# Kernel tuning notes

Hardware: AMD Instinct MI355X
Metric: run time of the kernel (lower is better)

The kernel has to match this reference:

```python
import jax, jax.numpy as jnp
import numpy as np

HIDDEN = 512
HEADS = 8


def setup_inputs() -> dict:
    key = jax.random.key(0)
    ks = jax.random.split(key, 7)
    B, S, D = 4, 2048, HIDDEN
    scale = 1.0 / np.sqrt(D)
    return {
        "src": jax.random.normal(ks[0], (B, S, D), dtype=jnp.float32),
        "Wq": jax.random.normal(ks[1], (D, D), dtype=jnp.float32) * scale,
        "bq": jax.random.normal(ks[2], (D,), dtype=jnp.float32) * 0.01,
        "Wk": jax.random.normal(ks[3], (D, D), dtype=jnp.float32) * scale,
        "bk": jax.random.normal(ks[4], (D,), dtype=jnp.float32) * 0.01,
        "Wv": jax.random.normal(ks[5], (D, D), dtype=jnp.float32) * scale,
        "bv": jax.random.normal(ks[6], (D,), dtype=jnp.float32) * 0.01,
    }


def reference(src, Wq, bq, Wk, bk, Wv, bv):
    B, S, D = src.shape
    H = HEADS
    hd = D // H
    # QKV projections -> [B, S, H, hd]
    q = (src @ Wq + bq).reshape(B, S, H, hd)
    k = (src @ Wk + bk).reshape(B, S, H, hd)
    v = (src @ Wv + bv).reshape(B, S, H, hd)
    # scores [B, H, S, S]; note: NO causal mask (matches original module)
    scores = jnp.einsum("bqhd,bkhd->bhqk", q, k) / jnp.sqrt(jnp.asarray(hd, src.dtype))
    attn = jax.nn.softmax(scores, axis=-1)
    out = jnp.einsum("bhqk,bkhd->bqhd", attn, v)
    return out.reshape(B, S, D)
```

## Files before the change

### kernel.cpp

```cpp
#include <hip/hip_runtime.h>

typedef __bf16 bf16;
typedef __bf16 bf16x8 __attribute__((ext_vector_type(8)));
typedef __bf16 bf16x4 __attribute__((ext_vector_type(4)));
typedef float f32x4 __attribute__((ext_vector_type(4)));
typedef float f32x16 __attribute__((ext_vector_type(16)));
typedef unsigned int u32;

#define QK_SCALE 0.1803368801111204f

__device__ __forceinline__ int swzb(int row, int col) {
    return (((row) << 7) + ((col) << 1)) ^ (((row) & 7) << 4);
}

__device__ __forceinline__ void gload_lds16(const void* g, void* l) {
    __builtin_amdgcn_global_load_lds(
        (const __attribute__((address_space(1))) unsigned int*)g,
        (__attribute__((address_space(3))) unsigned int*)l, 16, 0, 0);
}

__device__ __forceinline__ u32 cvtpk(float lo, float hi) {
    u32 r;
    asm("v_cvt_pk_bf16_f32 %0, %1, %2" : "=v"(r) : "v"(lo), "v"(hi));
    return r;
}

__device__ __forceinline__ void pl32swap(u32& a, u32& b) {
    asm("v_permlane32_swap_b32 %0, %1" : "+v"(a), "+v"(b));
}

__global__ __launch_bounds__(256) void cast_src(const float* __restrict__ x,
                                                bf16* __restrict__ y) {
    int i = blockIdx.x * 256 + threadIdx.x;
    float4 v = reinterpret_cast<const float4*>(x)[i];
    bf16x4 p;
    p[0] = (bf16)v.x; p[1] = (bf16)v.y; p[2] = (bf16)v.z; p[3] = (bf16)v.w;
    reinterpret_cast<bf16x4*>(y)[i] = p;
}

__global__ __launch_bounds__(256) void wtrans_all(const float* __restrict__ Wq,
                                                  const float* __restrict__ Wk,
                                                  const float* __restrict__ Wv,
                                                  bf16* __restrict__ Wt_all) {
    __shared__ float T[64][65];
    const int w = blockIdx.z;
    const float* W = w == 0 ? Wq : (w == 1 ? Wk : Wv);
    const float wsc = (w == 0) ? QK_SCALE : 1.0f;
    bf16* Wt = Wt_all + (size_t)w * 512 * 512;
    const int k0 = blockIdx.x * 64, n0 = blockIdx.y * 64;
    const int tx = threadIdx.x & 63, ty = threadIdx.x >> 6;
#pragma unroll
    for (int i = 0; i < 16; ++i) {
        int row = ty * 16 + i;
        T[row][tx] = W[(size_t)(k0 + row) * 512 + n0 + tx];
    }
    __syncthreads();
#pragma unroll
    for (int i = 0; i < 16; ++i) {
        int row = ty * 16 + i;
        Wt[(size_t)(n0 + row) * 512 + k0 + tx] = (bf16)(T[tx][row] * wsc);
    }
}

__global__ __launch_bounds__(256) void qkv_gemm_all(const bf16* __restrict__ srcb,
                                                    const bf16* __restrict__ Wt_all,
                                                    const float* __restrict__ bq,
                                                    const float* __restrict__ bk,
                                                    const float* __restrict__ bv,
                                                    bf16* __restrict__ Qb,
                                                    bf16* __restrict__ Kb,
                                                    bf16* __restrict__ Vtb) {
    __shared__ __align__(16) bf16 As[128 * 64];
    __shared__ __align__(16) bf16 Bs[128 * 64];
    const int t = threadIdx.x, lane = t & 63, wid = t >> 6;
    const int m0 = blockIdx.x * 128;
    const int n0g = blockIdx.y * 128;
    const int oi = n0g >> 9, n0 = n0g & 511;
    const float* bias = oi == 0 ? bq : (oi == 1 ? bk : bv);
    const float bsc = (oi == 0) ? QK_SCALE : 1.0f;
    bf16* outp = oi == 0 ? Qb : (oi == 1 ? Kb : Vtb);
    const bf16* Wt = Wt_all + (size_t)oi * 512 * 512;
    const bool sw = (oi == 2);
    const int wm = (wid >> 1) * 64, wn = (wid & 1) * 64;
    const int fr = lane & 15, fq = lane >> 4;

    f32x4 acc[4][4] = {};

    for (int k0 = 0; k0 < 512; k0 += 64) {
        __syncthreads();
#pragma unroll
        for (int c = 0; c < 4; ++c) {
            int u = (wid * 4 + c) * 64 + lane;
            int row = u >> 3;
            int slot = (u & 7) ^ (row & 7);
            gload_lds16(srcb + (size_t)(m0 + row) * 512 + k0 + slot * 8,
                        (char*)As + (wid * 4 + c) * 1024);
            gload_lds16(Wt + (size_t)(n0 + row) * 512 + k0 + slot * 8,
                        (char*)Bs + (wid * 4 + c) * 1024);
        }
        __syncthreads();

        bf16x8 a[2][4], b[2][4];
#pragma unroll
        for (int c = 0; c < 2; ++c)
#pragma unroll
            for (int i = 0; i < 4; ++i) {
                a[c][i] = *reinterpret_cast<const bf16x8*>(
                    (const char*)As + swzb(wm + i * 16 + fr, c * 32 + fq * 8));
                b[c][i] = *reinterpret_cast<const bf16x8*>(
                    (const char*)Bs + swzb(wn + i * 16 + fr, c * 32 + fq * 8));
            }
        if (!sw) {
#pragma unroll
            for (int i = 0; i < 4; ++i)
#pragma unroll
                for (int j = 0; j < 4; ++j)
#pragma unroll
                    for (int c = 0; c < 2; ++c)
                        acc[i][j] = __builtin_amdgcn_mfma_f32_16x16x32_bf16(a[c][i], b[c][j], acc[i][j], 0, 0, 0);
        } else {
#pragma unroll
            for (int i = 0; i < 4; ++i)
#pragma unroll
                for (int j = 0; j < 4; ++j)
#pragma unroll
                    for (int c = 0; c < 2; ++c)
                        acc[i][j] = __builtin_amdgcn_mfma_f32_16x16x32_bf16(b[c][j], a[c][i], acc[i][j], 0, 0, 0);
        }
    }

    if (!sw) {
#pragma unroll
        for (int j = 0; j < 4; ++j) {
            int n = n0 + wn + j * 16 + fr;
            float bj = bias[n] * bsc;
            int h = n >> 6, d = n & 63;
#pragma unroll
            for (int i = 0; i < 4; ++i)
#pragma unroll
                for (int r = 0; r < 4; ++r) {
                    int m = m0 + wm + i * 16 + fq * 4 + r;
                    int b_ = m >> 11, s = m & 2047;
                    outp[(((size_t)(b_ * 8 + h)) * 2048 + s) * 64 + d] =
                        (bf16)(acc[i][j][r] + bj);
                }
        }
    } else {
#pragma unroll
        for (int j = 0; j < 4; ++j)
#pragma unroll
            for (int r = 0; r < 4; ++r) {
                int n = n0 + wn + j * 16 + fq * 4 + r;
                float bj = bias[n];
                int h = n >> 6, d = n & 63;
#pragma unroll
                for (int i = 0; i < 4; ++i) {
                    int m = m0 + wm + i * 16 + fr;
                    int b_ = m >> 11, s = m & 2047;
                    outp[(((size_t)(b_ * 8 + h)) * 64 + d) * 2048 + s] =
                        (bf16)(acc[i][j][r] + bj);
                }
            }
    }
}

__global__ __launch_bounds__(256, 2) void attn_fwd(const bf16* __restrict__ Q,
                                                   const bf16* __restrict__ K,
                                                   const bf16* __restrict__ Vt,
                                                   float* __restrict__ out) {
    __shared__ __align__(16) bf16 Ks[2][64 * 64];
    __shared__ __align__(16) bf16 Vs[2][64 * 64];
    const int t = threadIdx.x, lane = t & 63, wid = t >> 6;
    const int c31 = lane & 31, h = lane >> 5;
    const int bh = blockIdx.y;
    const int qw = blockIdx.x * 128 + wid * 32;

    const bf16* Qp = Q + ((size_t)bh * 2048 + qw + c31) * 64;
    bf16x8 qf[4];
#pragma unroll
    for (int ks = 0; ks < 4; ++ks)
        qf[ks] = *reinterpret_cast<const bf16x8*>(&Qp[ks * 16 + h * 8]);

    bf16x8 bones;
#pragma unroll
    for (int e = 0; e < 8; ++e) bones[e] = (bf16)1.0f;

    f32x16 acc_o[2] = {};
    f32x16 acc_l = {};

    const char* Kpb0 = (const char*)(K + (size_t)bh * 2048 * 64);
    const char* Vpb0 = (const char*)(Vt + (size_t)bh * 64 * 2048);

    const int u0 = wid * 2 * 64 + lane, u1 = u0 + 64;
    const int row0 = u0 >> 3, slot0 = (u0 & 7) ^ (row0 & 7);
    const int row1 = u1 >> 3, slot1 = (u1 & 7) ^ (row1 & 7);

    auto stage = [&](int buf, int kv0) {
        const char* Kpb = Kpb0 + (size_t)kv0 * 128;
        const char* Vpb = Vpb0 + (size_t)kv0 * 2;
        gload_lds16(Kpb + row0 * 128 + slot0 * 16, (char*)Ks[buf] + (wid * 2 + 0) * 1024);
        gload_lds16(Kpb + row1 * 128 + slot1 * 16, (char*)Ks[buf] + (wid * 2 + 1) * 1024);
        gload_lds16(Vpb + (size_t)row0 * 4096 + slot0 * 16, (char*)Vs[buf] + (wid * 2 + 0) * 1024);
        gload_lds16(Vpb + (size_t)row1 * 4096 + slot1 * 16, (char*)Vs[buf] + (wid * 2 + 1) * 1024);
    };

    auto compute = [&](int buf) {
        f32x16 s[2] = {};
#pragma unroll
        for (int kt = 0; kt < 2; ++kt)
#pragma unroll
            for (int ks = 0; ks < 4; ++ks) {
                bf16x8 kf = *reinterpret_cast<const bf16x8*>(
                    (const char*)Ks[buf] + swzb(kt * 32 + c31, ks * 16 + h * 8));
                s[kt] = __builtin_amdgcn_mfma_f32_32x32x16_bf16(kf, qf[ks], s[kt], 0, 0, 0);
            }

#pragma unroll
        for (int kt = 0; kt < 2; ++kt)
#pragma unroll
            for (int r = 0; r < 16; ++r)
                s[kt][r] = exp2f(s[kt][r]);

        bf16x8 pa[4];
#pragma unroll
        for (int kt = 0; kt < 2; ++kt)
#pragma unroll
            for (int k2 = 0; k2 < 2; ++k2) {
                u32 X = cvtpk(s[kt][8 * k2 + 0], s[kt][8 * k2 + 1]);
                u32 Y = cvtpk(s[kt][8 * k2 + 4], s[kt][8 * k2 + 5]);
                u32 Z = cvtpk(s[kt][8 * k2 + 2], s[kt][8 * k2 + 3]);
                u32 W = cvtpk(s[kt][8 * k2 + 6], s[kt][8 * k2 + 7]);
                pl32swap(X, Y);
                pl32swap(Z, W);
                union { bf16x8 v; u32 w[4]; } pu;
                pu.w[0] = X; pu.w[1] = Z; pu.w[2] = Y; pu.w[3] = W;
                pa[kt * 2 + k2] = pu.v;
            }

#pragma unroll
        for (int kstep = 0; kstep < 4; ++kstep) {
#pragma unroll
            for (int dt = 0; dt < 2; ++dt) {
                bf16x8 vf = *reinterpret_cast<const bf16x8*>(
                    (const char*)Vs[buf] + swzb(dt * 32 + c31, kstep * 16 + h * 8));
                acc_o[dt] = __builtin_amdgcn_mfma_f32_32x32x16_bf16(pa[kstep], vf, acc_o[dt], 0, 0, 0);
            }
            acc_l = __builtin_amdgcn_mfma_f32_32x32x16_bf16(pa[kstep], bones, acc_l, 0, 0, 0);
        }
    };

    stage(0, 0);
    __syncthreads();

    for (int kv0 = 0; kv0 < 2048; kv0 += 128) {
        stage(1, kv0 + 64);
        compute(0);
        __syncthreads();
        if (kv0 + 128 < 2048) stage(0, kv0 + 128);
        compute(1);
        __syncthreads();
    }

    const int b_ = bh >> 3, hh = bh & 7;
#pragma unroll
    for (int reg = 0; reg < 16; ++reg) {
        float inv = __builtin_amdgcn_rcpf(acc_l[reg]);
        int qr = (reg & 3) + 8 * (reg >> 2) + 4 * h;
        int s_ = qw + qr;
        size_t base = ((size_t)b_ * 2048 + s_) * 512 + hh * 64;
        out[base + c31]      = acc_o[0][reg] * inv;
        out[base + 32 + c31] = acc_o[1][reg] * inv;
    }
}

extern "C" void kernel_launch(void* const* d_in, const int* in_sizes, int n_in,
                              void* d_out, int out_size, void* d_ws, size_t ws_size,
                              hipStream_t stream) {
    const float* src = (const float*)d_in[0];
    const float* Wq  = (const float*)d_in[1];
    const float* bq  = (const float*)d_in[2];
    const float* Wk  = (const float*)d_in[3];
    const float* bk  = (const float*)d_in[4];
    const float* Wv  = (const float*)d_in[5];
    const float* bv  = (const float*)d_in[6];
    float* out = (float*)d_out;

    char* ws = (char*)d_ws;
    const size_t WT_SZ  = 512u * 512u * sizeof(bf16);
    const size_t QKV_SZ = 8192u * 512u * sizeof(bf16);
    bf16* WtA  = (bf16*)(ws);
    bf16* srcb = (bf16*)(ws + 3 * WT_SZ);
    bf16* Qb   = (bf16*)(ws + 3 * WT_SZ + QKV_SZ);
    bf16* Kb   = (bf16*)(ws + 3 * WT_SZ + 2 * QKV_SZ);
    bf16* Vtb  = (bf16*)(ws + 3 * WT_SZ + 3 * QKV_SZ);

    cast_src<<<4096, 256, 0, stream>>>(src, srcb);
    wtrans_all<<<dim3(8, 8, 3), 256, 0, stream>>>(Wq, Wk, Wv, WtA);

    qkv_gemm_all<<<dim3(64, 12), 256, 0, stream>>>(srcb, WtA, bq, bk, bv, Qb, Kb, Vtb);

    attn_fwd<<<dim3(16, 32), 256, 0, stream>>>(Qb, Kb, Vtb, out);
}
```

Baseline: 94.93 us.

## Double KV tile per stage in attention and add MFMA priority hints

The attention kernel now stages 128 KV rows per buffer instead of 64, which halves the number of barriers and loop iterations. It adds a new XOR swizzle for the wider V tile (16-way over 256-byte rows). Inside compute, the two score tiles are interleaved and wrapped with s_setprio, and exp2 now uses the raw builtin. LDS use doubles to 64KB per block, which may limit occupancy at the 2 blocks per CU the launch bounds request.

```diff
diff --git a/kernel.cpp b/kernel.cpp
--- a/kernel.cpp
+++ b/kernel.cpp
@@ -12,6 +12,12 @@
 __device__ __forceinline__ int swzb(int row, int col) {
     return (((row) << 7) + ((col) << 1)) ^ (((row) & 7) << 4);
 }
+__device__ __forceinline__ int kswz(int row, int g) {
+    return row * 128 + ((g ^ (row & 7)) << 4);
+}
+__device__ __forceinline__ int vswz(int row, int g) {
+    return row * 256 + ((g ^ (row & 15)) << 4);
+}
 
 __device__ __forceinline__ void gload_lds16(const void* g, void* l) {
     __builtin_amdgcn_global_load_lds(
@@ -24,7 +30,6 @@
     asm("v_cvt_pk_bf16_f32 %0, %1, %2" : "=v"(r) : "v"(lo), "v"(hi));
     return r;
 }
-
 __device__ __forceinline__ void pl32swap(u32& a, u32& b) {
     asm("v_permlane32_swap_b32 %0, %1" : "+v"(a), "+v"(b));
 }
@@ -168,8 +173,8 @@
                                                    const bf16* __restrict__ K,
                                                    const bf16* __restrict__ Vt,
                                                    float* __restrict__ out) {
-    __shared__ __align__(16) bf16 Ks[2][64 * 64];
-    __shared__ __align__(16) bf16 Vs[2][64 * 64];
+    __shared__ __align__(16) bf16 Ks[2][128 * 64];
+    __shared__ __align__(16) bf16 Vs[2][64 * 128];
     const int t = threadIdx.x, lane = t & 63, wid = t >> 6;
     const int c31 = lane & 31, h = lane >> 5;
     const int bh = blockIdx.y;
@@ -191,72 +196,91 @@
     const char* Kpb0 = (const char*)(K + (size_t)bh * 2048 * 64);
     const char* Vpb0 = (const char*)(Vt + (size_t)bh * 64 * 2048);
 
-    const int u0 = wid * 2 * 64 + lane, u1 = u0 + 64;
-    const int row0 = u0 >> 3, slot0 = (u0 & 7) ^ (row0 & 7);
-    const int row1 = u1 >> 3, slot1 = (u1 & 7) ^ (row1 & 7);
+    int koffs[4], voffs[4];
+#pragma unroll
+    for (int c = 0; c < 4; ++c) {
+        int cc = wid * 4 + c;
+        int kr = cc * 8 + (lane >> 3);
+        koffs[c] = kr * 128 + (((lane & 7) ^ (kr & 7)) << 4);
+        int d = cc * 4 + (lane >> 4);
+        voffs[c] = d * 4096 + (((lane & 15) ^ (d & 15)) << 4);
+    }
 
     auto stage = [&](int buf, int kv0) {
-        const char* Kpb = Kpb0 + (size_t)kv0 * 128;
-        const char* Vpb = Vpb0 + (size_t)kv0 * 2;
-        gload_lds16(Kpb + row0 * 128 + slot0 * 16, (char*)Ks[buf] + (wid * 2 + 0) * 1024);
-        gload_lds16(Kpb + row1 * 128 + slot1 * 16, (char*)Ks[buf] + (wid * 2 + 1) * 1024);
-        gload_lds16(Vpb + (size_t)row0 * 4096 + slot0 * 16, (char*)Vs[buf] + (wid * 2 + 0) * 1024);
-        gload_lds16(Vpb + (size_t)row1 * 4096 + slot1 * 16, (char*)Vs[buf] + (wid * 2 + 1) * 1024);
+#pragma unroll
+        for (int c = 0; c < 4; ++c)
+            gload_lds16(Kpb0 + (size_t)kv0 * 128 + koffs[c],
+                        (char*)Ks[buf] + (wid * 4 + c) * 1024);
+#pragma unroll
+        for (int c = 0; c < 4; ++c)
+            gload_lds16(Vpb0 + (size_t)kv0 * 2 + voffs[c],
+                        (char*)Vs[buf] + (wid * 4 + c) * 1024);
     };
 
     auto compute = [&](int buf) {
-        f32x16 s[2] = {};
-#pragma unroll
-        for (int kt = 0; kt < 2; ++kt)
+#pragma unroll
+        for (int p = 0; p < 2; ++p) {
+            f32x16 s0 = {}, s1 = {};
+            __builtin_amdgcn_s_setprio(1);
 #pragma unroll
             for (int ks = 0; ks < 4; ++ks) {
-                bf16x8 kf = *reinterpret_cast<const bf16x8*>(
-                    (const char*)Ks[buf] + swzb(kt * 32 + c31, ks * 16 + h * 8));
-                s[kt] = __builtin_amdgcn_mfma_f32_32x32x16_bf16(kf, qf[ks], s[kt], 0, 0, 0);
-            }
-
-#pragma unroll
-        for (int kt = 0; kt < 2; ++kt)
-#pragma unroll
-            for (int r = 0; r < 16; ++r)
-                s[kt][r] = exp2f(s[kt][r]);
-
-        bf16x8 pa[4];
-#pragma unroll
-        for (int kt = 0; kt < 2; ++kt)
-#pragma unroll
-            for (int k2 = 0; k2 < 2; ++k2) {
-                u32 X = cvtpk(s[kt][8 * k2 + 0], s[kt][8 * k2 + 1]);
-                u32 Y = cvtpk(s[kt][8 * k2 + 4], s[kt][8 * k2 + 5]);
-                u32 Z = cvtpk(s[kt][8 * k2 + 2], s[kt][8 * k2 + 3]);
-                u32 W = cvtpk(s[kt][8 * k2 + 6], s[kt][8 * k2 + 7]);
-                pl32swap(X, Y);
-                pl32swap(Z, W);
-                union { bf16x8 v; u32 w[4]; } pu;
-                pu.w[0] = X; pu.w[1] = Z; pu.w[2] = Y; pu.w[3] = W;
-                pa[kt * 2 + k2] = pu.v;
-            }
-
-#pragma unroll
-        for (int kstep = 0; kstep < 4; ++kstep) {
-#pragma unroll
-            for (int dt = 0; dt < 2; ++dt) {
-                bf16x8 vf = *reinterpret_cast<const bf16x8*>(
-                    (const char*)Vs[buf] + swzb(dt * 32 + c31, kstep * 16 + h * 8));
-                acc_o[dt] = __builtin_amdgcn_mfma_f32_32x32x16_bf16(pa[kstep], vf, acc_o[dt], 0, 0, 0);
-            }
-            acc_l = __builtin_amdgcn_mfma_f32_32x32x16_bf16(pa[kstep], bones, acc_l, 0, 0, 0);
+                bf16x8 kf0 = *reinterpret_cast<const bf16x8*>(
+                    (const char*)Ks[buf] + kswz(p * 64 + c31, ks * 2 + h));
+                s0 = __builtin_amdgcn_mfma_f32_32x32x16_bf16(kf0, qf[ks], s0, 0, 0, 0);
+                bf16x8 kf1 = *reinterpret_cast<const bf16x8*>(
+                    (const char*)Ks[buf] + kswz(p * 64 + 32 + c31, ks * 2 + h));
+                s1 = __builtin_amdgcn_mfma_f32_32x32x16_bf16(kf1, qf[ks], s1, 0, 0, 0);
+            }
+            __builtin_amdgcn_s_setprio(0);
+
+#pragma unroll
+            for (int r = 0; r < 16; ++r) {
+                s0[r] = __builtin_amdgcn_exp2f(s0[r]);
+                s1[r] = __builtin_amdgcn_exp2f(s1[r]);
+            }
+
+            bf16x8 pa[4];
+#pragma unroll
+            for (int ktl = 0; ktl < 2; ++ktl) {
+                const f32x16& sv = ktl ? s1 : s0;
+#pragma unroll
+                for (int k2 = 0; k2 < 2; ++k2) {
+                    u32 X = cvtpk(sv[8 * k2 + 0], sv[8 * k2 + 1]);
+                    u32 Y = cvtpk(sv[8 * k2 + 4], sv[8 * k2 + 5]);
+                    u32 Z = cvtpk(sv[8 * k2 + 2], sv[8 * k2 + 3]);
+                    u32 W = cvtpk(sv[8 * k2 + 6], sv[8 * k2 + 7]);
+                    pl32swap(X, Y);
+                    pl32swap(Z, W);
+                    union { bf16x8 v; u32 w[4]; } pu;
+                    pu.w[0] = X; pu.w[1] = Z; pu.w[2] = Y; pu.w[3] = W;
+                    pa[ktl * 2 + k2] = pu.v;
+                }
+            }
+
+            __builtin_amdgcn_s_setprio(1);
+#pragma unroll
+            for (int k2 = 0; k2 < 4; ++k2) {
+                int kg = p * 4 + k2;
+                bf16x8 vf0 = *reinterpret_cast<const bf16x8*>(
+                    (const char*)Vs[buf] + vswz(c31, kg * 2 + h));
+                acc_o[0] = __builtin_amdgcn_mfma_f32_32x32x16_bf16(pa[k2], vf0, acc_o[0], 0, 0, 0);
+                bf16x8 vf1 = *reinterpret_cast<const bf16x8*>(
+                    (const char*)Vs[buf] + vswz(32 + c31, kg * 2 + h));
+                acc_o[1] = __builtin_amdgcn_mfma_f32_32x32x16_bf16(pa[k2], vf1, acc_o[1], 0, 0, 0);
+                acc_l = __builtin_amdgcn_mfma_f32_32x32x16_bf16(pa[k2], bones, acc_l, 0, 0, 0);
+            }
+            __builtin_amdgcn_s_setprio(0);
         }
     };
 
     stage(0, 0);
     __syncthreads();
 
-    for (int kv0 = 0; kv0 < 2048; kv0 += 128) {
-        stage(1, kv0 + 64);
+    for (int kv0 = 0; kv0 < 2048; kv0 += 256) {
+        stage(1, kv0 + 128);
         compute(0);
         __syncthreads();
-        if (kv0 + 128 < 2048) stage(0, kv0 + 128);
+        if (kv0 + 256 < 2048) stage(0, kv0 + 256);
         compute(1);
         __syncthreads();
     }
```

After: 80.02 us. 15.7% less time.
